# Performance work log

Hardware: AMD Instinct MI355X
Metric: run time of the kernel (lower is better)

## Reference

```python
import jax, jax.numpy as jnp
import numpy as np

BS = 8  # JPEG block size

LUMINANCE_QUANTIZATION_TABLE = np.array((
    (16, 11, 10, 16, 24, 40, 51, 61),
    (12, 12, 14, 19, 26, 58, 60, 55),
    (14, 13, 16, 24, 40, 57, 69, 56),
    (14, 17, 22, 29, 51, 87, 80, 62),
    (18, 22, 37, 56, 68, 109, 103, 77),
    (24, 36, 55, 64, 81, 104, 113, 92),
    (49, 64, 78, 87, 103, 121, 120, 101),
    (72, 92, 95, 98, 112, 100, 103, 99)), dtype=np.float64)
Q_TABLE = (LUMINANCE_QUANTIZATION_TABLE / 100.0).astype(np.float32)  # matches process_Q_table


def _dct_matrix(N):
    # Orthonormal DCT-II matrix C[k, n] = f_k * cos(pi*(2n+1)*k/(2N)),
    # identical math to grid_factors * cos(DCT_freq_grid * (2*DCT_arange + 1)) in the torch code
    n = np.arange(N)[None, :]
    k = np.arange(N)[:, None]
    C = np.cos(np.pi * (2 * n + 1) * k / (2.0 * N))
    f = np.full((N, 1), np.sqrt(2.0 / N))
    f[0, 0] = 1.0 / np.sqrt(N)
    return (f * C).astype(np.float32)

_DCT_MAT = _dct_matrix(BS)


def setup_inputs() -> dict:
    key = jax.random.key(0)
    k1, k2 = jax.random.split(key)
    image = jax.random.uniform(k1, (16, 1, 1024, 1024), dtype=jnp.float32) * 255.0
    quality_factor = jax.random.uniform(k2, (16,), dtype=jnp.float32, minval=10.0, maxval=90.0)
    return {"image": image, "quality_factor": quality_factor}


def reference(image, quality_factor):
    B, _, H, W = image.shape
    hb, wb = H // BS, W // BS
    # Image_2_Blocks: [B,1,H,W] -> [B, 8, 8, hb, wb]
    blocks = image.reshape(B, hb, BS, wb, BS).transpose(0, 2, 4, 1, 3)
    blocks = blocks - 128.0
    C = jnp.asarray(_DCT_MAT)
    # Blocks_DCT: orthonormal 2D DCT-II over the two 8-dims (axes 1 and 2)
    out = jnp.einsum('kn,bnmhw->bkmhw', C, blocks)
    out = jnp.einsum('lm,bkmhw->bklhw', C, out)
    # Set_QF factor: 5000/QF if QF<50 else 200-2*QF
    factor = jnp.where(quality_factor < 50.0, 5000.0 / quality_factor, 200.0 - 2.0 * quality_factor)
    factor = factor.reshape(B, 1, 1, 1, 1)
    Q = jnp.asarray(Q_TABLE).reshape(1, BS, BS, 1, 1)
    out = out / (factor * Q)
    # downsample_and_quantize=False -> no rounding
    return out.reshape(B, BS * BS, hb, wb)
```

## Files before the change

### kernel.cpp

```cpp
#include <hip/hip_runtime.h>
#include <hip/hip_bf16.h>


#define BS 8
#define HPIX 1024
#define WPIX 1024
#define HB (HPIX / BS)
#define WB (WPIX / BS)
#define BATCH 16

constexpr float DCT[8][8] = {
  { 0.35355339059327373f,  0.35355339059327373f,  0.35355339059327373f,  0.35355339059327373f,
    0.35355339059327373f,  0.35355339059327373f,  0.35355339059327373f,  0.35355339059327373f },
  { 0.49039264020161522f,  0.41573480615127262f,  0.27778511650980114f,  0.09754516100806413f,
   -0.09754516100806413f, -0.27778511650980114f, -0.41573480615127262f, -0.49039264020161522f },
  { 0.46193976625564337f,  0.19134171618254492f, -0.19134171618254492f, -0.46193976625564337f,
   -0.46193976625564337f, -0.19134171618254492f,  0.19134171618254492f,  0.46193976625564337f },
  { 0.41573480615127262f, -0.09754516100806413f, -0.49039264020161522f, -0.27778511650980114f,
    0.27778511650980114f,  0.49039264020161522f,  0.09754516100806413f, -0.41573480615127262f },
  { 0.35355339059327373f, -0.35355339059327373f, -0.35355339059327373f,  0.35355339059327373f,
    0.35355339059327373f, -0.35355339059327373f, -0.35355339059327373f,  0.35355339059327373f },
  { 0.27778511650980114f, -0.49039264020161522f,  0.09754516100806413f,  0.41573480615127262f,
   -0.41573480615127262f, -0.09754516100806413f,  0.49039264020161522f, -0.27778511650980114f },
  { 0.19134171618254492f, -0.46193976625564337f,  0.46193976625564337f, -0.19134171618254492f,
   -0.19134171618254492f,  0.46193976625564337f, -0.46193976625564337f,  0.19134171618254492f },
  { 0.09754516100806413f, -0.27778511650980114f,  0.41573480615127262f, -0.49039264020161522f,
    0.49039264020161522f, -0.41573480615127262f,  0.27778511650980114f, -0.09754516100806413f },
};

constexpr float INVQ[8][8] = {
  { 6.25f,              9.09090909090909f,  10.0f,              6.25f,
    4.16666666666667f,  2.5f,               1.96078431372549f,  1.63934426229508f },
  { 8.33333333333333f,  8.33333333333333f,  7.14285714285714f,  5.26315789473684f,
    3.84615384615385f,  1.72413793103448f,  1.66666666666667f,  1.81818181818182f },
  { 7.14285714285714f,  7.69230769230769f,  6.25f,              4.16666666666667f,
    2.5f,               1.75438596491228f,  1.44927536231884f,  1.78571428571429f },
  { 7.14285714285714f,  5.88235294117647f,  4.54545454545455f,  3.44827586206897f,
    1.96078431372549f,  1.14942528735632f,  1.25f,              1.61290322580645f },
  { 5.55555555555556f,  4.54545454545455f,  2.70270270270270f,  1.78571428571429f,
    1.47058823529412f,  0.91743119266055f,  0.970873786407767f, 1.29870129870130f },
  { 4.16666666666667f,  2.77777777777778f,  1.81818181818182f,  1.5625f,
    1.23456790123457f,  0.961538461538462f, 0.884955752212389f, 1.08695652173913f },
  { 2.04081632653061f,  1.5625f,            1.28205128205128f,  1.14942528735632f,
    0.970873786407767f, 0.826446280991736f, 0.833333333333333f, 0.990099009900990f },
  { 1.38888888888889f,  1.08695652173913f,  1.05263157894737f,  1.02040816326531f,
    0.892857142857143f, 1.0f,               0.970873786407767f, 1.01010101010101f },
};

__global__ __launch_bounds__(256) void jpeg_dct_q_kernel(
    const float* __restrict__ img,
    const float* __restrict__ qf,
    float* __restrict__ out)
{
    const int tid = blockIdx.x * blockDim.x + threadIdx.x;
    const int w = tid & (WB - 1);
    const int h = (tid >> 7) & (HB - 1);
    const int b = tid >> 14;

    const float* rowbase = img + ((size_t)b << 20) + (size_t)(h * BS) * WPIX + (size_t)(w * BS);

    float tmp[8][8];
#pragma unroll
    for (int k = 0; k < 8; ++k)
#pragma unroll
        for (int m = 0; m < 8; ++m)
            tmp[k][m] = 0.0f;

#pragma unroll
    for (int n = 0; n < 8; ++n) {
        const float4* p = reinterpret_cast<const float4*>(rowbase + n * WPIX);
        float4 a = p[0];
        float4 c = p[1];
        float r[8];
        r[0] = a.x - 128.0f; r[1] = a.y - 128.0f; r[2] = a.z - 128.0f; r[3] = a.w - 128.0f;
        r[4] = c.x - 128.0f; r[5] = c.y - 128.0f; r[6] = c.z - 128.0f; r[7] = c.w - 128.0f;
#pragma unroll
        for (int k = 0; k < 8; ++k) {
            const float cf = DCT[k][n];
#pragma unroll
            for (int m = 0; m < 8; ++m)
                tmp[k][m] = fmaf(cf, r[m], tmp[k][m]);
        }
    }

    const float q = qf[b];
    const float factor = (q < 50.0f) ? (5000.0f / q) : (200.0f - 2.0f * q);
    const float rf = 1.0f / factor;

    float* obase = out + ((size_t)b << 20) + (size_t)h * WB + (size_t)w;
#pragma unroll
    for (int k = 0; k < 8; ++k) {
#pragma unroll
        for (int l = 0; l < 8; ++l) {
            float s = 0.0f;
#pragma unroll
            for (int m = 0; m < 8; ++m)
                s = fmaf(DCT[l][m], tmp[k][m], s);
            s = s * rf * INVQ[k][l];
            obase[(size_t)(k * 8 + l) * (HB * WB)] = s;
        }
    }
}

extern "C" void kernel_launch(void* const* d_in, const int* in_sizes, int n_in,
                              void* d_out, int out_size, void* d_ws, size_t ws_size,
                              hipStream_t stream) {
    const float* img = (const float*)d_in[0];
    const float* qf  = (const float*)d_in[1];
    float* out = (float*)d_out;

    const int total_blocks = BATCH * HB * WB;
    const int block = 256;
    const int grid = total_blocks / block;

    jpeg_dct_q_kernel<<<grid, block, 0, stream>>>(img, qf, out);
}
```

Before: 112.9 us.

## Stage DCT outputs in LDS double buffer for float4 coalesced stores

Each thread now writes its per-frequency results into a double-buffered shared-memory tile covering two block rows, then threads cooperatively read float4 vectors and emit 128-bit stores per output plane. The goal is to replace the scalar 4-byte strided stores with wide vector stores. Launch bounds add a minimum-blocks hint of 4 to push occupancy. It adds eight __syncthreads per block and LDS traffic. The two-buffer scheme relies on the barrier ordering to avoid overwrite races.

Result: no change. 111.3 us (-1.5%).

```diff
diff --git a/kernel.cpp b/kernel.cpp
--- a/kernel.cpp
+++ b/kernel.cpp
@@ -47,15 +47,20 @@
     0.892857142857143f, 1.0f,               0.970873786407767f, 1.01010101010101f },
 };
 
-__global__ __launch_bounds__(256) void jpeg_dct_q_kernel(
+__global__ __launch_bounds__(256, 4) void jpeg_dct_q_kernel(
     const float* __restrict__ img,
     const float* __restrict__ qf,
     float* __restrict__ out)
 {
-    const int tid = blockIdx.x * blockDim.x + threadIdx.x;
-    const int w = tid & (WB - 1);
-    const int h = (tid >> 7) & (HB - 1);
-    const int b = tid >> 14;
+    __shared__ float lds[2][2][8][WB];
+
+    const int t = threadIdx.x;
+    const int g = blockIdx.x;
+    const int b = g >> 6;
+    const int h0 = (g & 63) << 1;
+    const int w = t & (WB - 1);
+    const int hsub = t >> 7;
+    const int h = h0 + hsub;
 
     const float* rowbase = img + ((size_t)b << 20) + (size_t)(h * BS) * WPIX + (size_t)(w * BS);
 
@@ -87,17 +92,30 @@
     const float factor = (q < 50.0f) ? (5000.0f / q) : (200.0f - 2.0f * q);
     const float rf = 1.0f / factor;
 
-    float* obase = out + ((size_t)b << 20) + (size_t)h * WB + (size_t)w;
+    const int p_hsub = t >> 7;
+    const int p_l = (t >> 4) & 7;
+    const int p_g0 = t & 15;
+    const size_t obatch = (size_t)b << 20;
+
 #pragma unroll
     for (int k = 0; k < 8; ++k) {
+        const int buf = k & 1;
 #pragma unroll
         for (int l = 0; l < 8; ++l) {
             float s = 0.0f;
 #pragma unroll
             for (int m = 0; m < 8; ++m)
                 s = fmaf(DCT[l][m], tmp[k][m], s);
-            s = s * rf * INVQ[k][l];
-            obase[(size_t)(k * 8 + l) * (HB * WB)] = s;
+            lds[buf][hsub][l][w] = s * rf * INVQ[k][l];
+        }
+        __syncthreads();
+#pragma unroll
+        for (int it = 0; it < 2; ++it) {
+            const int grp = p_g0 + 16 * it;
+            float4 v = *reinterpret_cast<const float4*>(&lds[buf][p_hsub][p_l][4 * grp]);
+            float* dst = out + obatch + (size_t)(k * 8 + p_l) * (HB * WB)
+                             + (size_t)(h0 + p_hsub) * WB + 4 * grp;
+            *reinterpret_cast<float4*>(dst) = v;
         }
     }
 }
@@ -109,9 +127,8 @@
     const float* qf  = (const float*)d_in[1];
     float* out = (float*)d_out;
 
-    const int total_blocks = BATCH * HB * WB;
+    const int grid = BATCH * (HB / 2);
     const int block = 256;
-    const int grid = total_blocks / block;
 
     jpeg_dct_q_kernel<<<grid, block, 0, stream>>>(img, qf, out);
 }
```

## Split DCT across 8 threads per block using LDS transposes and vectorized stores

Applied to the files above, without the earlier changes.

Each thread previously computed a whole 8x8 DCT block, holding 64 accumulators and writing 64 scalar strided outputs. Now each workgroup handles 32 blocks in one block row, and each thread owns one column and then one row. The two 1D passes are exchanged through padded LDS buffers with barriers, and outputs are staged so each channel is written as coalesced float4 stores. The -128 shift is folded into the DC coefficient. This targets register pressure and uncoalesced stores, at the cost of LDS traffic and two __syncthreads per workgroup.

Result: no change. 111.5 us (-1.3%).

```diff
diff --git a/kernel.cpp b/kernel.cpp
--- a/kernel.cpp
+++ b/kernel.cpp
@@ -8,6 +8,9 @@
 #define HB (HPIX / BS)
 #define WB (WPIX / BS)
 #define BATCH 16
+
+#define S_A 9
+#define S_B 33
 
 constexpr float DCT[8][8] = {
   { 0.35355339059327373f,  0.35355339059327373f,  0.35355339059327373f,  0.35355339059327373f,
@@ -47,58 +50,84 @@
     0.892857142857143f, 1.0f,               0.970873786407767f, 1.01010101010101f },
 };
 
-__global__ __launch_bounds__(256) void jpeg_dct_q_kernel(
+__global__ __launch_bounds__(256, 8) void jpeg_dct_q_kernel(
     const float* __restrict__ img,
     const float* __restrict__ qf,
     float* __restrict__ out)
 {
-    const int tid = blockIdx.x * blockDim.x + threadIdx.x;
-    const int w = tid & (WB - 1);
-    const int h = (tid >> 7) & (HB - 1);
-    const int b = tid >> 14;
+    __shared__ float ldsA[32 * 8 * S_A];
+    __shared__ float ldsB[64 * S_B];
+    __shared__ float lds_invq[64];
 
-    const float* rowbase = img + ((size_t)b << 20) + (size_t)(h * BS) * WPIX + (size_t)(w * BS);
+    const int t  = threadIdx.x;
+    const int wg = blockIdx.x;
+    const int b  = wg >> 9;
+    const int h  = (wg >> 2) & 127;
+    const int w0 = (wg & 3) << 5;
+    const int m   = t & 7;
+    const int blk = t >> 3;
 
-    float tmp[8][8];
+    if (t == 0) {
 #pragma unroll
-    for (int k = 0; k < 8; ++k)
+        for (int ch = 0; ch < 64; ++ch)
+            lds_invq[ch] = INVQ[ch >> 3][ch & 7];
+    }
+
+    const float* colbase = img + ((size_t)b << 20)
+                               + (size_t)(h * BS) * WPIX
+                               + (size_t)((w0 + blk) * BS + m);
+    float pix[8];
 #pragma unroll
-        for (int m = 0; m < 8; ++m)
-            tmp[k][m] = 0.0f;
+    for (int n = 0; n < 8; ++n)
+        pix[n] = colbase[(size_t)n * WPIX];
 
 #pragma unroll
-    for (int n = 0; n < 8; ++n) {
-        const float4* p = reinterpret_cast<const float4*>(rowbase + n * WPIX);
-        float4 a = p[0];
-        float4 c = p[1];
-        float r[8];
-        r[0] = a.x - 128.0f; r[1] = a.y - 128.0f; r[2] = a.z - 128.0f; r[3] = a.w - 128.0f;
-        r[4] = c.x - 128.0f; r[5] = c.y - 128.0f; r[6] = c.z - 128.0f; r[7] = c.w - 128.0f;
+    for (int k = 0; k < 8; ++k) {
+        float s = 0.0f;
 #pragma unroll
-        for (int k = 0; k < 8; ++k) {
-            const float cf = DCT[k][n];
+        for (int n = 0; n < 8; ++n)
+            s = fmaf(DCT[k][n], pix[n], s);
+        if (k == 0) s -= 362.03867196751236f;
+        ldsA[(blk * 8 + m) * S_A + k] = s;
+    }
+    __syncthreads();
+
+    const int j = t & 7;
+    float tt[8];
 #pragma unroll
-            for (int m = 0; m < 8; ++m)
-                tmp[k][m] = fmaf(cf, r[m], tmp[k][m]);
-        }
+    for (int mm = 0; mm < 8; ++mm)
+        tt[mm] = ldsA[(blk * 8 + mm) * S_A + j];
+#pragma unroll
+    for (int l = 0; l < 8; ++l) {
+        float s = 0.0f;
+#pragma unroll
+        for (int mm = 0; mm < 8; ++mm)
+            s = fmaf(DCT[l][mm], tt[mm], s);
+        ldsB[(j * 8 + l) * S_B + blk] = s;
     }
+    __syncthreads();
 
     const float q = qf[b];
     const float factor = (q < 50.0f) ? (5000.0f / q) : (200.0f - 2.0f * q);
     const float rf = 1.0f / factor;
 
-    float* obase = out + ((size_t)b << 20) + (size_t)h * WB + (size_t)w;
 #pragma unroll
-    for (int k = 0; k < 8; ++k) {
-#pragma unroll
-        for (int l = 0; l < 8; ++l) {
-            float s = 0.0f;
-#pragma unroll
-            for (int m = 0; m < 8; ++m)
-                s = fmaf(DCT[l][m], tmp[k][m], s);
-            s = s * rf * INVQ[k][l];
-            obase[(size_t)(k * 8 + l) * (HB * WB)] = s;
-        }
+    for (int it = 0; it < 2; ++it) {
+        const int g   = t + 256 * it;
+        const int ch  = g >> 3;
+        const int grp = g & 7;
+        const float qsc = rf * lds_invq[ch];
+        const float* src = &ldsB[ch * S_B + 4 * grp];
+        float4 v;
+        v.x = src[0] * qsc;
+        v.y = src[1] * qsc;
+        v.z = src[2] * qsc;
+        v.w = src[3] * qsc;
+        float* dst = out + ((size_t)b << 20)
+                         + (size_t)ch * (HB * WB)
+                         + (size_t)h * WB
+                         + (size_t)(w0 + 4 * grp);
+        *reinterpret_cast<float4*>(dst) = v;
     }
 }
 
@@ -109,9 +138,8 @@
     const float* qf  = (const float*)d_in[1];
     float* out = (float*)d_out;
 
-    const int total_blocks = BATCH * HB * WB;
+    const int grid = BATCH * HB * 4;
     const int block = 256;
-    const int grid = total_blocks / block;
 
     jpeg_dct_q_kernel<<<grid, block, 0, stream>>>(img, qf, out);
 }
```

## Split each DCT block across two threads and stage outputs in LDS for float4 stores

Applied to the files above, without the earlier changes.

Each 8x8 block is now handled by two threads, each loading a 4-column half, with the second-stage partial sums combined through a lane shuffle. Results are written to a 64x256 LDS tile and then stored as coalesced float4 rows, where before each thread issued scalar stores strided across channels. The -128 offset is folded into the DC term as a constant correction. This adds a 64KB LDS allocation and a barrier per workgroup, which limits occupancy, and the constant correction may change rounding slightly.

Result: slower. 136.7 us (+21.0%).

```diff
diff --git a/kernel.cpp b/kernel.cpp
--- a/kernel.cpp
+++ b/kernel.cpp
@@ -47,58 +47,97 @@
     0.892857142857143f, 1.0f,               0.970873786407767f, 1.01010101010101f },
 };
 
-__global__ __launch_bounds__(256) void jpeg_dct_q_kernel(
+__global__ __launch_bounds__(512, 4) void jpeg_dct_q_kernel(
     const float* __restrict__ img,
     const float* __restrict__ qf,
     float* __restrict__ out)
 {
-    const int tid = blockIdx.x * blockDim.x + threadIdx.x;
-    const int w = tid & (WB - 1);
-    const int h = (tid >> 7) & (HB - 1);
-    const int b = tid >> 14;
+    __shared__ float ldsB[64][256];
 
-    const float* rowbase = img + ((size_t)b << 20) + (size_t)(h * BS) * WPIX + (size_t)(w * BS);
+    const int t  = threadIdx.x;
+    const int wg = blockIdx.x;
+    const int b  = wg >> 6;
+    const int h0 = (wg & 63) << 1;
+    const int blk  = t >> 1;
+    const int half = t & 1;
+    const int hs = blk >> 7;
+    const int w  = blk & 127;
 
-    float tmp[8][8];
+    const float* base = img + ((size_t)b << 20)
+                            + (size_t)((h0 + hs) * BS) * WPIX
+                            + (size_t)(w * BS + half * 4);
+    float4 pix[8];
+#pragma unroll
+    for (int n = 0; n < 8; ++n)
+        pix[n] = *reinterpret_cast<const float4*>(base + (size_t)n * WPIX);
+
+    float T[8][4];
 #pragma unroll
     for (int k = 0; k < 8; ++k)
 #pragma unroll
-        for (int m = 0; m < 8; ++m)
-            tmp[k][m] = 0.0f;
-
+        for (int j = 0; j < 4; ++j)
+            T[k][j] = 0.0f;
 #pragma unroll
     for (int n = 0; n < 8; ++n) {
-        const float4* p = reinterpret_cast<const float4*>(rowbase + n * WPIX);
-        float4 a = p[0];
-        float4 c = p[1];
-        float r[8];
-        r[0] = a.x - 128.0f; r[1] = a.y - 128.0f; r[2] = a.z - 128.0f; r[3] = a.w - 128.0f;
-        r[4] = c.x - 128.0f; r[5] = c.y - 128.0f; r[6] = c.z - 128.0f; r[7] = c.w - 128.0f;
+        const float* pr = reinterpret_cast<const float*>(&pix[n]);
+        float r0 = pr[0], r1 = pr[1], r2 = pr[2], r3 = pr[3];
 #pragma unroll
         for (int k = 0; k < 8; ++k) {
             const float cf = DCT[k][n];
-#pragma unroll
-            for (int m = 0; m < 8; ++m)
-                tmp[k][m] = fmaf(cf, r[m], tmp[k][m]);
+            T[k][0] = fmaf(cf, r0, T[k][0]);
+            T[k][1] = fmaf(cf, r1, T[k][1]);
+            T[k][2] = fmaf(cf, r2, T[k][2]);
+            T[k][3] = fmaf(cf, r3, T[k][3]);
         }
     }
+#pragma unroll
+    for (int j = 0; j < 4; ++j)
+        T[0][j] -= 362.03867196751236f;
+
+    float cf[8][4];
+#pragma unroll
+    for (int l = 0; l < 8; ++l)
+#pragma unroll
+        for (int j = 0; j < 4; ++j)
+            cf[l][j] = half ? DCT[l][4 + j] : DCT[l][j];
 
     const float q = qf[b];
     const float factor = (q < 50.0f) ? (5000.0f / q) : (200.0f - 2.0f * q);
     const float rf = 1.0f / factor;
 
-    float* obase = out + ((size_t)b << 20) + (size_t)h * WB + (size_t)w;
 #pragma unroll
     for (int k = 0; k < 8; ++k) {
+        float p[8];
 #pragma unroll
         for (int l = 0; l < 8; ++l) {
             float s = 0.0f;
 #pragma unroll
-            for (int m = 0; m < 8; ++m)
-                s = fmaf(DCT[l][m], tmp[k][m], s);
-            s = s * rf * INVQ[k][l];
-            obase[(size_t)(k * 8 + l) * (HB * WB)] = s;
+            for (int j = 0; j < 4; ++j)
+                s = fmaf(cf[l][j], T[k][j], s);
+            p[l] = s;
         }
+        float fs[8];
+#pragma unroll
+        for (int l = 0; l < 8; ++l)
+            fs[l] = p[l] + __shfl_xor(p[l], 1, 64);
+#pragma unroll
+        for (int i = 0; i < 4; ++i) {
+            const float v  = half ? fs[4 + i] : fs[i];
+            const float iq = half ? INVQ[k][4 + i] : INVQ[k][i];
+            const int ch = k * 8 + half * 4 + i;
+            ldsB[ch][blk] = v * rf * iq;
+        }
+    }
+    __syncthreads();
+
+    const int lane = t & 63;
+    const int wv   = t >> 6;
+    float* outbase = out + ((size_t)b << 20) + (size_t)(h0 * WB) + (size_t)(lane * 4);
+#pragma unroll
+    for (int s = 0; s < 8; ++s) {
+        const int ch = wv * 8 + s;
+        const float4 v = *reinterpret_cast<const float4*>(&ldsB[ch][lane * 4]);
+        *reinterpret_cast<float4*>(outbase + (size_t)ch * (HB * WB)) = v;
     }
 }
 
@@ -109,9 +148,8 @@
     const float* qf  = (const float*)d_in[1];
     float* out = (float*)d_out;
 
-    const int total_blocks = BATCH * HB * WB;
-    const int block = 256;
-    const int grid = total_blocks / block;
+    const int grid = BATCH * (HB / 2);
+    const int block = 512;
 
     jpeg_dct_q_kernel<<<grid, block, 0, stream>>>(img, qf, out);
 }
```
